# Kernel tuning notes

Hardware: AMD Instinct MI355X
Metric: run time of the kernel (lower is better)

Reference implementation:

```python
import jax, jax.numpy as jnp
import numpy as np

L = 4096
B = 8192

def setup_inputs() -> dict:
    key = jax.random.key(0)
    k1, k2 = jax.random.split(key)
    X = jax.random.normal(k1, (B, L), dtype=jnp.float32)
    # lengths in [1, L] so every row has at least one valid element
    N = jax.random.randint(k2, (B, 1), 1, L + 1, dtype=jnp.int32)
    return {"X": X, "N": N}

def reference(X, N):
    # mask[i, j] = j < N[i, 0]
    mask = (jnp.arange(X.shape[1])[None, :] < N).astype(X.dtype)  # [B, L]
    neg_inf = jnp.array(-jnp.inf, dtype=X.dtype)
    # row max over valid entries only
    max_X = jnp.max(jnp.where(mask > 0, X, neg_inf), axis=1, keepdims=True)  # [B, 1]
    exp_X = jnp.exp(X - max_X)  # computed over all entries, as in original
    sum_exp_X = jnp.sum(exp_X * mask, axis=1, keepdims=True)  # [B, 1]
    return mask * exp_X / sum_exp_X
```

## Files before the change

kernel.cpp:

```cpp
#include <hip/hip_runtime.h>
#include <math.h>

#define ROW_LEN 4096
#define NROWS   8192
#define BLOCK   256
#define V4_PER_THREAD 4

__global__ __launch_bounds__(BLOCK) void masked_softmax_kernel(
    const float* __restrict__ X,
    const int* __restrict__ N,
    float* __restrict__ out)
{
    const int row = blockIdx.x;
    const int tid = threadIdx.x;
    const int n   = N[row];

    const float4* __restrict__ Xr = (const float4*)(X + (size_t)row * ROW_LEN);
    float4* __restrict__ Or       = (float4*)(out + (size_t)row * ROW_LEN);

    float4 v[V4_PER_THREAD];
    float m = -INFINITY;
    #pragma unroll
    for (int i = 0; i < V4_PER_THREAD; i++) {
        const int idx = i * BLOCK + tid;
        v[i] = Xr[idx];
        const int col = idx * 4;
        if (col + 0 < n) m = fmaxf(m, v[i].x);
        if (col + 1 < n) m = fmaxf(m, v[i].y);
        if (col + 2 < n) m = fmaxf(m, v[i].z);
        if (col + 3 < n) m = fmaxf(m, v[i].w);
    }

    #pragma unroll
    for (int off = 32; off > 0; off >>= 1)
        m = fmaxf(m, __shfl_down(m, off, 64));

    __shared__ float s_red[4];
    const int wave = tid >> 6;
    const int lane = tid & 63;
    if (lane == 0) s_red[wave] = m;
    __syncthreads();
    if (tid == 0) {
        s_red[0] = fmaxf(fmaxf(s_red[0], s_red[1]), fmaxf(s_red[2], s_red[3]));
    }
    __syncthreads();
    m = s_red[0];
    __syncthreads();

    float s = 0.0f;
    #pragma unroll
    for (int i = 0; i < V4_PER_THREAD; i++) {
        const int idx = i * BLOCK + tid;
        const int col = idx * 4;
        v[i].x = __expf(v[i].x - m);
        v[i].y = __expf(v[i].y - m);
        v[i].z = __expf(v[i].z - m);
        v[i].w = __expf(v[i].w - m);
        if (col + 0 < n) s += v[i].x;
        if (col + 1 < n) s += v[i].y;
        if (col + 2 < n) s += v[i].z;
        if (col + 3 < n) s += v[i].w;
    }

    #pragma unroll
    for (int off = 32; off > 0; off >>= 1)
        s += __shfl_down(s, off, 64);
    if (lane == 0) s_red[wave] = s;
    __syncthreads();
    if (tid == 0) {
        s_red[0] = (s_red[0] + s_red[1]) + (s_red[2] + s_red[3]);
    }
    __syncthreads();
    const float inv = 1.0f / s_red[0];

    #pragma unroll
    for (int i = 0; i < V4_PER_THREAD; i++) {
        const int idx = i * BLOCK + tid;
        const int col = idx * 4;
        float4 o;
        o.x = (col + 0 < n) ? v[i].x * inv : 0.0f;
        o.y = (col + 1 < n) ? v[i].y * inv : 0.0f;
        o.z = (col + 2 < n) ? v[i].z * inv : 0.0f;
        o.w = (col + 3 < n) ? v[i].w * inv : 0.0f;
        Or[idx] = o;
    }
}

extern "C" void kernel_launch(void* const* d_in, const int* in_sizes, int n_in,
                              void* d_out, int out_size, void* d_ws, size_t ws_size,
                              hipStream_t stream) {
    const float* X = (const float*)d_in[0];
    const int*   N = (const int*)d_in[1];
    float* out = (float*)d_out;
    masked_softmax_kernel<<<NROWS, BLOCK, 0, stream>>>(X, N, out);
}
```

Baseline: 229.7 us.

## Map one wavefront per row and use nontemporal loads and stores

Each row is now handled by a single 64-lane wavefront holding 16 float4 per lane, so the max and sum reductions become pure cross-lane shuffles with no shared memory or block barriers. Global loads and stores use nontemporal builtins to avoid cache pollution on a streaming workload, and the row length is made wave-uniform with readfirstlane. The cost is much higher register pressure per lane (64 floats live), which may lower occupancy, and fewer loads in flight per row.

```diff
diff --git a/kernel.cpp b/kernel.cpp
--- a/kernel.cpp
+++ b/kernel.cpp
@@ -4,85 +4,73 @@
 #define ROW_LEN 4096
 #define NROWS   8192
 #define BLOCK   256
-#define V4_PER_THREAD 4
+#define WAVES_PER_BLOCK (BLOCK / 64)
+#define F4_PER_LANE 16
 
-__global__ __launch_bounds__(BLOCK) void masked_softmax_kernel(
+typedef float vf4 __attribute__((ext_vector_type(4)));
+
+__global__ __launch_bounds__(BLOCK) void masked_softmax_wave(
     const float* __restrict__ X,
     const int* __restrict__ N,
     float* __restrict__ out)
 {
-    const int row = blockIdx.x;
-    const int tid = threadIdx.x;
-    const int n   = N[row];
+    const int wave = threadIdx.x >> 6;
+    const int lane = threadIdx.x & 63;
+    const int row  = blockIdx.x * WAVES_PER_BLOCK + wave;
 
-    const float4* __restrict__ Xr = (const float4*)(X + (size_t)row * ROW_LEN);
-    float4* __restrict__ Or       = (float4*)(out + (size_t)row * ROW_LEN);
+    const int n = __builtin_amdgcn_readfirstlane(N[row]);
 
-    float4 v[V4_PER_THREAD];
+    const vf4* __restrict__ Xr = (const vf4*)(X + (size_t)row * ROW_LEN);
+    vf4* __restrict__ Or       = (vf4*)(out + (size_t)row * ROW_LEN);
+
+    vf4 v[F4_PER_LANE];
+    #pragma unroll
+    for (int j = 0; j < F4_PER_LANE; j++) {
+        v[j] = __builtin_nontemporal_load(&Xr[lane + 64 * j]);
+    }
+
     float m = -INFINITY;
     #pragma unroll
-    for (int i = 0; i < V4_PER_THREAD; i++) {
-        const int idx = i * BLOCK + tid;
-        v[i] = Xr[idx];
-        const int col = idx * 4;
-        if (col + 0 < n) m = fmaxf(m, v[i].x);
-        if (col + 1 < n) m = fmaxf(m, v[i].y);
-        if (col + 2 < n) m = fmaxf(m, v[i].z);
-        if (col + 3 < n) m = fmaxf(m, v[i].w);
+    for (int j = 0; j < F4_PER_LANE; j++) {
+        const int col = 4 * (lane + 64 * j);
+        m = fmaxf(m, (col + 0 < n) ? v[j].x : -INFINITY);
+        m = fmaxf(m, (col + 1 < n) ? v[j].y : -INFINITY);
+        m = fmaxf(m, (col + 2 < n) ? v[j].z : -INFINITY);
+        m = fmaxf(m, (col + 3 < n) ? v[j].w : -INFINITY);
     }
-
     #pragma unroll
-    for (int off = 32; off > 0; off >>= 1)
-        m = fmaxf(m, __shfl_down(m, off, 64));
-
-    __shared__ float s_red[4];
-    const int wave = tid >> 6;
-    const int lane = tid & 63;
-    if (lane == 0) s_red[wave] = m;
-    __syncthreads();
-    if (tid == 0) {
-        s_red[0] = fmaxf(fmaxf(s_red[0], s_red[1]), fmaxf(s_red[2], s_red[3]));
-    }
-    __syncthreads();
-    m = s_red[0];
-    __syncthreads();
+    for (int off = 1; off < 64; off <<= 1)
+        m = fmaxf(m, __shfl_xor(m, off, 64));
 
     float s = 0.0f;
     #pragma unroll
-    for (int i = 0; i < V4_PER_THREAD; i++) {
-        const int idx = i * BLOCK + tid;
-        const int col = idx * 4;
-        v[i].x = __expf(v[i].x - m);
-        v[i].y = __expf(v[i].y - m);
-        v[i].z = __expf(v[i].z - m);
-        v[i].w = __expf(v[i].w - m);
-        if (col + 0 < n) s += v[i].x;
-        if (col + 1 < n) s += v[i].y;
-        if (col + 2 < n) s += v[i].z;
-        if (col + 3 < n) s += v[i].w;
+    for (int j = 0; j < F4_PER_LANE; j++) {
+        const int col = 4 * (lane + 64 * j);
+        float ex = __expf(v[j].x - m);
+        float ey = __expf(v[j].y - m);
+        float ez = __expf(v[j].z - m);
+        float ew = __expf(v[j].w - m);
+        ex = (col + 0 < n) ? ex : 0.0f;
+        ey = (col + 1 < n) ? ey : 0.0f;
+        ez = (col + 2 < n) ? ez : 0.0f;
+        ew = (col + 3 < n) ? ew : 0.0f;
+        v[j].x = ex; v[j].y = ey; v[j].z = ez; v[j].w = ew;
+        s += (ex + ey) + (ez + ew);
     }
+    #pragma unroll
+    for (int off = 1; off < 64; off <<= 1)
+        s += __shfl_xor(s, off, 64);
+
+    const float inv = 1.0f / s;
 
     #pragma unroll
-    for (int off = 32; off > 0; off >>= 1)
-        s += __shfl_down(s, off, 64);
-    if (lane == 0) s_red[wave] = s;
-    __syncthreads();
-    if (tid == 0) {
-        s_red[0] = (s_red[0] + s_red[1]) + (s_red[2] + s_red[3]);
-    }
-    __syncthreads();
-    const float inv = 1.0f / s_red[0];
-
-    #pragma unroll
-    for (int i = 0; i < V4_PER_THREAD; i++) {
-        const int idx = i * BLOCK + tid;
-        const int col = idx * 4;
-        float4 o;
-        o.x = (col + 0 < n) ? v[i].x * inv : 0.0f;
-        o.y = (col + 1 < n) ? v[i].y * inv : 0.0f;
-        o.z = (col + 2 < n) ? v[i].z * inv : 0.0f;
-        o.w = (col + 3 < n) ? v[i].w * inv : 0.0f;
-        Or[idx] = o;
+    for (int j = 0; j < F4_PER_LANE; j++) {
+        vf4 o;
+        o.x = v[j].x * inv;
+        o.y = v[j].y * inv;
+        o.z = v[j].z * inv;
+        o.w = v[j].w * inv;
+        __builtin_nontemporal_store(o, &Or[lane + 64 * j]);
     }
 }
 
@@ -92,5 +80,5 @@
     const float* X = (const float*)d_in[0];
     const int*   N = (const int*)d_in[1];
     float* out = (float*)d_out;
-    masked_softmax_kernel<<<NROWS, BLOCK, 0, stream>>>(X, N, out);
+    masked_softmax_wave<<<NROWS / WAVES_PER_BLOCK, BLOCK, 0, stream>>>(X, N, out);
 }
```

Measured after the change: 223.3 us. 1.03x faster.
